# Kernel optimization log

Hardware: AMD Instinct MI355X
Metric: run time of the kernel (lower is better)

Reference implementation:

```python
import jax, jax.numpy as jnp
import numpy as np

TEMPERATURE = 0.03


def setup_inputs() -> dict:
    key = jax.random.key(0)
    k1, k2, k3 = jax.random.split(key, 3)
    B, d = 8192, 256
    z_a = jax.random.normal(k1, (B, d), dtype=jnp.float32)
    z_t = jax.random.normal(k2, (B, d), dtype=jnp.float32)
    # module expects L2-normalized projections
    z_a = z_a / jnp.linalg.norm(z_a, axis=-1, keepdims=True)
    z_t = z_t / jnp.linalg.norm(z_t, axis=-1, keepdims=True)
    patient_ids = jax.random.randint(k3, (B,), 0, 2048, dtype=jnp.int64)
    return {"z_a": z_a, "z_t": z_t, "patient_ids": patient_ids}


def _direction_loss(sim, cross_mask):
    # sim: (B, B) row i = anchor i vs all candidates; cross_mask: (B, B) valid negatives
    B = sim.shape[0]
    pos = jnp.diagonal(sim)                              # (B,) positive logits
    logit_mask = cross_mask | jnp.eye(B, dtype=bool)     # negatives + the positive
    lse = jax.nn.logsumexp(sim, axis=1, where=logit_mask)  # (B,)
    row_loss = lse - pos                                 # CE with label = positive
    valid = cross_mask.any(axis=1)                       # rows with >=1 cross-patient neg
    cnt = jnp.sum(valid)
    total = jnp.sum(jnp.where(valid, row_loss, 0.0))
    return jnp.where(cnt > 0, total / jnp.maximum(cnt, 1).astype(sim.dtype), 0.0)


def reference(z_a, z_t, patient_ids):
    sim = jnp.matmul(z_a, z_t.T) / TEMPERATURE           # (B, B)
    cross = patient_ids[:, None] != patient_ids[None, :] # cross-patient negative mask
    loss_a2t = _direction_loss(sim, cross)
    loss_t2a = _direction_loss(sim.T, cross.T)
    return (loss_a2t + loss_t2a) / 2.0
```

## Files before the change

kernel.cpp:

```cpp
#include <hip/hip_runtime.h>
#include <math.h>

#define BSZ    8192
#define DDIM   256
#define SCALE  33.33333333333333f
#define C_OFF  34.0f
#define SC_L2E 48.08983470f
#define C2     49.05163139f

typedef float floatx4 __attribute__((ext_vector_type(4)));
typedef long long fp8x8;

__device__ __forceinline__ fp8x8 cvt8_f8(const float* __restrict__ g)
{
    const float4 lo = *(const float4*)g;
    const float4 hi = *(const float4*)(g + 4);
    int a = __builtin_amdgcn_cvt_pk_fp8_f32(lo.x, lo.y, 0, false);
    a     = __builtin_amdgcn_cvt_pk_fp8_f32(lo.z, lo.w, a, true);
    int b = __builtin_amdgcn_cvt_pk_fp8_f32(hi.x, hi.y, 0, false);
    b     = __builtin_amdgcn_cvt_pk_fp8_f32(hi.z, hi.w, b, true);
    int2 r; r.x = a; r.y = b;
    return *(fp8x8*)&r;
}

__global__ __launch_bounds__(256) void prep_kernel(
    const float* __restrict__ za, const float* __restrict__ zt,
    unsigned char* __restrict__ za_f8, unsigned char* __restrict__ zt_perm,
    float* __restrict__ zbase)
{
    const int bid = blockIdx.x, tid = threadIdx.x;
    if (bid < 1024) {
        const int i = (bid * 256 + tid) * 8;
        *(fp8x8*)(za_f8 + i) = cvt8_f8(za + i);
        if (bid < 16) {
            const int z = bid * 1024 + tid * 4;
            *(float4*)&zbase[z] = (float4){0.f, 0.f, 0.f, 0.f};
            if (bid == 0 && tid == 0) {
                zbase[16384] = 0.f;
                ((int*)zbase)[16385] = 0;
                ((int*)zbase)[16386] = 0;
            }
        }
    } else {
        const int S     = (bid - 1024) * 256 + tid;
        const int chunk = S >> 9, P = S & 511;
        const int col   = P >> 2, sp = P & 3;
        const int sl    = sp ^ ((col >> 2) & 3);
        const int cb    = chunk >> 3, kc = chunk & 7;
        const float* src = zt + (size_t)(cb * 128 + col) * DDIM + kc * 32 + sl * 8;
        *(fp8x8*)(zt_perm + (size_t)S * 8) = cvt8_f8(src);
    }
}

__global__ __launch_bounds__(256, 2) void sim_fused(
    const unsigned char* __restrict__ za_f8, const unsigned char* __restrict__ zt_perm,
    const int* __restrict__ pid,
    float* __restrict__ s_row, float* __restrict__ s_col,
    float* __restrict__ posv)
{
    __shared__ __align__(16) unsigned char Bs[2][4096];
    __shared__ int   pidc[512];
    __shared__ float colsum[512];

    const int bid   = blockIdx.x;
    const int strip = bid & 15, band = bid >> 4;
    const int row0  = band * 128, scol0 = strip * 512;
    const int tid   = threadIdx.x, lane = tid & 63, wid = tid >> 6;
    const int q     = lane >> 4, lc = lane & 15;
    const int rbase = row0 + wid * 32;
    const int qs8   = (q ^ ((lc >> 2) & 3)) * 8;

    pidc[tid]         = pid[scol0 + tid];
    pidc[tid + 256]   = pid[scol0 + tid + 256];
    colsum[tid]       = 0.f;
    colsum[tid + 256] = 0.f;

    fp8x8 af[2][8];
    #pragma unroll
    for (int m = 0; m < 2; m++) {
        const unsigned char* ga = za_f8 + (size_t)(rbase + m * 16 + lc) * DDIM + q * 8;
        #pragma unroll
        for (int kc = 0; kc < 8; kc++)
            af[m][kc] = *(const fp8x8*)(ga + kc * 32);
    }

    int prw[2][4];
    #pragma unroll
    for (int m = 0; m < 2; m++)
        #pragma unroll
        for (int r = 0; r < 4; r++)
            prw[m][r] = pid[rbase + m * 16 + q * 4 + r];

    const unsigned char* zp = zt_perm + (size_t)(strip * 32) * 4096
                            + wid * 1024 + lane * 16;

#define STAGE(g, b)                                                              \
    do {                                                                         \
        const unsigned char* _s = zp + (size_t)(g) * 4096;                       \
        unsigned char* _d = &Bs[b][0] + wid * 1024;                              \
        __builtin_amdgcn_global_load_lds(                                        \
            (const __attribute__((address_space(1))) void*)_s,                   \
            (__attribute__((address_space(3))) void*)_d, 16, 0, 0);              \
    } while (0)

    STAGE(0, 0);

    float rowp[8] = {0.f, 0.f, 0.f, 0.f, 0.f, 0.f, 0.f, 0.f};
    const int diag_t = (row0 - scol0) >> 7;

    for (int t = 0; t < 4; t++) {
        floatx4 acc[2][8];
        #pragma unroll
        for (int m = 0; m < 2; m++)
            #pragma unroll
            for (int n = 0; n < 8; n++)
                acc[m][n] = (floatx4){0.f, 0.f, 0.f, 0.f};

        #pragma unroll
        for (int kc = 0; kc < 8; kc++) {
            __syncthreads();
            const int g = t * 8 + kc;
            if (g + 1 < 32) STAGE(g + 1, (g + 1) & 1);

            const unsigned char* B = &Bs[g & 1][0];
            fp8x8 bfr[8];
            #pragma unroll
            for (int n = 0; n < 8; n++)
                bfr[n] = *(const fp8x8*)(B + (n * 16 + lc) * 32 + qs8);

            #pragma unroll
            for (int m = 0; m < 2; m++)
                #pragma unroll
                for (int n = 0; n < 8; n++)
                    acc[m][n] = __builtin_amdgcn_mfma_f32_16x16x32_fp8_fp8(
                        af[m][kc], bfr[n], acc[m][n], 0, 0, 0);
        }

        int pc[8];
        #pragma unroll
        for (int n = 0; n < 8; n++) pc[n] = pidc[t * 128 + n * 16 + lc];

        float colp[8] = {0.f, 0.f, 0.f, 0.f, 0.f, 0.f, 0.f, 0.f};
        #pragma unroll
        for (int m = 0; m < 2; m++) {
            #pragma unroll
            for (int r = 0; r < 4; r++) {
                const int pr = prw[m][r];
                float rsum = 0.f;
                #pragma unroll
                for (int n = 0; n < 8; n++) {
                    float e = __builtin_amdgcn_exp2f(fmaf(acc[m][n][r], SC_L2E, -C2));
                    e = (pr != pc[n]) ? e : 0.f;
                    rsum += e;
                    colp[n] += e;
                }
                rowp[m * 4 + r] += rsum;
            }
        }

        if (t == diag_t) {
            #pragma unroll
            for (int m = 0; m < 2; m++) {
                const int nstar = wid * 2 + m;
                #pragma unroll
                for (int r = 0; r < 4; r++) {
                    float v = 0.f;
                    #pragma unroll
                    for (int n = 0; n < 8; n++)
                        v = (n == nstar) ? acc[m][n][r] : v;
                    float e = __builtin_amdgcn_exp2f(fmaf(v, SC_L2E, -C2));
                    const bool own = (lc == q * 4 + r);
                    e = own ? e : 0.f;
                    rowp[m * 4 + r] += e;
                    #pragma unroll
                    for (int n = 0; n < 8; n++)
                        colp[n] += (n == nstar) ? e : 0.f;
                    if (own) posv[rbase + m * 16 + q * 4 + r] = v * SCALE;
                }
            }
        }

        #pragma unroll
        for (int n = 0; n < 8; n++) {
            colp[n] += __shfl_xor(colp[n], 16, 64);
            colp[n] += __shfl_xor(colp[n], 32, 64);
        }
        if (q == 0) {
            #pragma unroll
            for (int n = 0; n < 8; n++)
                atomicAdd(&colsum[t * 128 + n * 16 + lc], colp[n]);
        }
    }

    #pragma unroll
    for (int i = 0; i < 8; i++) {
        rowp[i] += __shfl_xor(rowp[i], 1, 64);
        rowp[i] += __shfl_xor(rowp[i], 2, 64);
        rowp[i] += __shfl_xor(rowp[i], 4, 64);
        rowp[i] += __shfl_xor(rowp[i], 8, 64);
    }
    float rw = rowp[0];
    #pragma unroll
    for (int idx = 1; idx < 8; idx++)
        rw = (lc == idx) ? rowp[idx] : rw;
    if (lc < 8)
        atomicAdd(&s_row[rbase + (lc >> 2) * 16 + q * 4 + (lc & 3)], rw);

    __syncthreads();
    atomicAdd(&s_col[scol0 + tid], colsum[tid]);
    atomicAdd(&s_col[scol0 + tid + 256], colsum[tid + 256]);
#undef STAGE
}

__global__ __launch_bounds__(256) void finalize_rows(
    const int* __restrict__ pid,
    const float* __restrict__ s_row, const float* __restrict__ s_col,
    const float* __restrict__ posv,
    float* __restrict__ total, int* __restrict__ flag, int* __restrict__ cnt,
    float* __restrict__ out)
{
    const int i = blockIdx.x * 256 + threadIdx.x;
    const float p = posv[i];
    const float c = (logf(s_row[i]) + C_OFF - p)
                  + (logf(s_col[i]) + C_OFF - p);

    float v = c;
    #pragma unroll
    for (int off = 32; off > 0; off >>= 1) v += __shfl_down(v, off, 64);
    if ((threadIdx.x & 63) == 0) atomicAdd(total, v);

    const unsigned long long m = __ballot(pid[i] != pid[0]);
    if (m != 0ull && (threadIdx.x & 63) == 0) atomicOr(flag, 1);

    __syncthreads();
    __threadfence();
    if (threadIdx.x == 0) {
        const int done = atomicAdd(cnt, 1);
        if (done == (int)gridDim.x - 1) {
            const float t = atomicAdd(total, 0.0f);
            const int   f = atomicOr(flag, 0);
            out[0] = f ? t / (2.0f * (float)BSZ) : 0.0f;
        }
    }
}

extern "C" void kernel_launch(void* const* d_in, const int* in_sizes, int n_in,
                              void* d_out, int out_size, void* d_ws, size_t ws_size,
                              hipStream_t stream)
{
    const float* za  = (const float*)d_in[0];
    const float* zt  = (const float*)d_in[1];
    const int*   pid = (const int*)d_in[2];
    float* out = (float*)d_out;

    unsigned char* za_f8   = (unsigned char*)d_ws;
    unsigned char* zt_perm = za_f8 + (size_t)BSZ * DDIM;
    float*  s_row   = (float*)(zt_perm + (size_t)BSZ * DDIM);
    float*  s_col   = s_row + BSZ;
    float*  total   = s_col + BSZ;
    int*    flag    = (int*)(total + 1);
    int*    cnt     = flag + 1;
    float*  posv    = (float*)(cnt + 1);

    prep_kernel<<<dim3(2048), 256, 0, stream>>>(za, zt, za_f8, zt_perm, s_row);

    sim_fused<<<dim3(1024), 256, 0, stream>>>(za_f8, zt_perm, pid,
                                              s_row, s_col, posv);

    finalize_rows<<<dim3(BSZ / 256), 256, 0, stream>>>(
        pid, s_row, s_col, posv, total, flag, cnt, out);
}
```

Baseline: 125.4 us.

## Convert z_a to fp8 in-kernel and halve sync count with larger LDS stages

Drops the z_a fp8 conversion from the prep kernel: the main kernel now loads fp32 z_a rows and converts them to fp8 in registers, so the prep grid shrinks to the z_t permutation. The LDS double buffer doubles in size so each stage carries two k-chunks, cutting the number of __syncthreads barriers per tile in half. In exchange, each of the 16 strip blocks per band converts the same fp32 rows redundantly and reads four times more bytes for A, and LDS use per block grows.

```diff
diff --git a/kernel.cpp b/kernel.cpp
--- a/kernel.cpp
+++ b/kernel.cpp
@@ -24,41 +24,36 @@
 }
 
 __global__ __launch_bounds__(256) void prep_kernel(
-    const float* __restrict__ za, const float* __restrict__ zt,
-    unsigned char* __restrict__ za_f8, unsigned char* __restrict__ zt_perm,
+    const float* __restrict__ zt, unsigned char* __restrict__ zt_perm,
     float* __restrict__ zbase)
 {
     const int bid = blockIdx.x, tid = threadIdx.x;
-    if (bid < 1024) {
-        const int i = (bid * 256 + tid) * 8;
-        *(fp8x8*)(za_f8 + i) = cvt8_f8(za + i);
-        if (bid < 16) {
-            const int z = bid * 1024 + tid * 4;
-            *(float4*)&zbase[z] = (float4){0.f, 0.f, 0.f, 0.f};
-            if (bid == 0 && tid == 0) {
-                zbase[16384] = 0.f;
-                ((int*)zbase)[16385] = 0;
-                ((int*)zbase)[16386] = 0;
-            }
-        }
-    } else {
-        const int S     = (bid - 1024) * 256 + tid;
-        const int chunk = S >> 9, P = S & 511;
-        const int col   = P >> 2, sp = P & 3;
-        const int sl    = sp ^ ((col >> 2) & 3);
-        const int cb    = chunk >> 3, kc = chunk & 7;
-        const float* src = zt + (size_t)(cb * 128 + col) * DDIM + kc * 32 + sl * 8;
-        *(fp8x8*)(zt_perm + (size_t)S * 8) = cvt8_f8(src);
+    const int S     = bid * 256 + tid;
+    const int chunk = S >> 9, P = S & 511;
+    const int col   = P >> 2, sp = P & 3;
+    const int sl    = sp ^ ((col >> 2) & 3);
+    const int cb    = chunk >> 3, kc = chunk & 7;
+    const float* src = zt + (size_t)(cb * 128 + col) * DDIM + kc * 32 + sl * 8;
+    *(fp8x8*)(zt_perm + (size_t)S * 8) = cvt8_f8(src);
+
+    if (bid < 16) {
+        const int z = bid * 1024 + tid * 4;
+        *(float4*)&zbase[z] = (float4){0.f, 0.f, 0.f, 0.f};
+        if (bid == 0 && tid == 0) {
+            zbase[16384] = 0.f;
+            ((int*)zbase)[16385] = 0;
+            ((int*)zbase)[16386] = 0;
+        }
     }
 }
 
 __global__ __launch_bounds__(256, 2) void sim_fused(
-    const unsigned char* __restrict__ za_f8, const unsigned char* __restrict__ zt_perm,
+    const float* __restrict__ za, const unsigned char* __restrict__ zt_perm,
     const int* __restrict__ pid,
     float* __restrict__ s_row, float* __restrict__ s_col,
     float* __restrict__ posv)
 {
-    __shared__ __align__(16) unsigned char Bs[2][4096];
+    __shared__ __align__(16) unsigned char Bs[2][8192];
     __shared__ int   pidc[512];
     __shared__ float colsum[512];
 
@@ -78,10 +73,10 @@
     fp8x8 af[2][8];
     #pragma unroll
     for (int m = 0; m < 2; m++) {
-        const unsigned char* ga = za_f8 + (size_t)(rbase + m * 16 + lc) * DDIM + q * 8;
+        const float* ga = za + (size_t)(rbase + m * 16 + lc) * DDIM + q * 8;
         #pragma unroll
         for (int kc = 0; kc < 8; kc++)
-            af[m][kc] = *(const fp8x8*)(ga + kc * 32);
+            af[m][kc] = cvt8_f8(ga + kc * 32);
     }
 
     int prw[2][4];
@@ -94,13 +89,16 @@
     const unsigned char* zp = zt_perm + (size_t)(strip * 32) * 4096
                             + wid * 1024 + lane * 16;
 
-#define STAGE(g, b)                                                              \
+#define STAGE(C, b)                                                              \
     do {                                                                         \
-        const unsigned char* _s = zp + (size_t)(g) * 4096;                       \
+        const unsigned char* _s = zp + (size_t)(C) * 8192;                       \
         unsigned char* _d = &Bs[b][0] + wid * 1024;                              \
         __builtin_amdgcn_global_load_lds(                                        \
             (const __attribute__((address_space(1))) void*)_s,                   \
             (__attribute__((address_space(3))) void*)_d, 16, 0, 0);              \
+        __builtin_amdgcn_global_load_lds(                                        \
+            (const __attribute__((address_space(1))) void*)(_s + 4096),          \
+            (__attribute__((address_space(3))) void*)(_d + 4096), 16, 0, 0);     \
     } while (0)
 
     STAGE(0, 0);
@@ -117,23 +115,27 @@
                 acc[m][n] = (floatx4){0.f, 0.f, 0.f, 0.f};
 
         #pragma unroll
-        for (int kc = 0; kc < 8; kc++) {
+        for (int c2 = 0; c2 < 4; c2++) {
             __syncthreads();
-            const int g = t * 8 + kc;
-            if (g + 1 < 32) STAGE(g + 1, (g + 1) & 1);
-
-            const unsigned char* B = &Bs[g & 1][0];
-            fp8x8 bfr[8];
-            #pragma unroll
-            for (int n = 0; n < 8; n++)
-                bfr[n] = *(const fp8x8*)(B + (n * 16 + lc) * 32 + qs8);
-
-            #pragma unroll
-            for (int m = 0; m < 2; m++)
+            const int C = t * 4 + c2;
+            if (C + 1 < 16) STAGE(C + 1, (C + 1) & 1);
+
+            const unsigned char* B = &Bs[C & 1][0];
+            #pragma unroll
+            for (int j = 0; j < 2; j++) {
+                const int kc = c2 * 2 + j;
+                fp8x8 bfr[8];
                 #pragma unroll
                 for (int n = 0; n < 8; n++)
-                    acc[m][n] = __builtin_amdgcn_mfma_f32_16x16x32_fp8_fp8(
-                        af[m][kc], bfr[n], acc[m][n], 0, 0, 0);
+                    bfr[n] = *(const fp8x8*)(B + j * 4096 + (n * 16 + lc) * 32 + qs8);
+
+                #pragma unroll
+                for (int m = 0; m < 2; m++)
+                    #pragma unroll
+                    for (int n = 0; n < 8; n++)
+                        acc[m][n] = __builtin_amdgcn_mfma_f32_16x16x32_fp8_fp8(
+                            af[m][kc], bfr[n], acc[m][n], 0, 0, 0);
+            }
         }
 
         int pc[8];
@@ -253,8 +255,7 @@
     const int*   pid = (const int*)d_in[2];
     float* out = (float*)d_out;
 
-    unsigned char* za_f8   = (unsigned char*)d_ws;
-    unsigned char* zt_perm = za_f8 + (size_t)BSZ * DDIM;
+    unsigned char* zt_perm = (unsigned char*)d_ws;
     float*  s_row   = (float*)(zt_perm + (size_t)BSZ * DDIM);
     float*  s_col   = s_row + BSZ;
     float*  total   = s_col + BSZ;
@@ -262,9 +263,9 @@
     int*    cnt     = flag + 1;
     float*  posv    = (float*)(cnt + 1);
 
-    prep_kernel<<<dim3(2048), 256, 0, stream>>>(za, zt, za_f8, zt_perm, s_row);
-
-    sim_fused<<<dim3(1024), 256, 0, stream>>>(za_f8, zt_perm, pid,
+    prep_kernel<<<dim3(1024), 256, 0, stream>>>(zt, zt_perm, s_row);
+
+    sim_fused<<<dim3(1024), 256, 0, stream>>>(za, zt_perm, pid,
                                               s_row, s_col, posv);
 
     finalize_rows<<<dim3(BSZ / 256), 256, 0, stream>>>(
```

After: 127.6 us. Within noise of the previous version (+1.7%).
